# Kernel tuning notes

Hardware: AMD Instinct MI355X
Metric: run time of the kernel (lower is better)

## Reference

```python
import jax, jax.numpy as jnp
import numpy as np

B, L, D = 4, 2048, 256
H, DH, MLP, MAX_REL = 8, 32, 1024, 16
LN_EPS = 1e-5


def _layernorm(x, g, b):
    mu = jnp.mean(x, axis=-1, keepdims=True)
    var = jnp.mean(jnp.square(x - mu), axis=-1, keepdims=True)
    return (x - mu) * jax.lax.rsqrt(var + LN_EPS) * g + b


def setup_inputs() -> dict:
    key = jax.random.key(0)
    ks = jax.random.split(key, 16)
    s = 0.02
    return {
        "x": jax.random.normal(ks[0], (B, L, D), jnp.float32),
        "key_padding_mask": jax.random.randint(ks[1], (B, L), 0, 2).astype(bool),
        "Wqkv": jax.random.normal(ks[2], (D, 3 * D), jnp.float32) * s,
        "bqkv": jnp.zeros((3 * D,), jnp.float32),
        "Wo": jax.random.normal(ks[3], (D, D), jnp.float32) * s,
        "bo": jnp.zeros((D,), jnp.float32),
        "ln1_g": jnp.ones((D,), jnp.float32),
        "ln1_b": jnp.zeros((D,), jnp.float32),
        "W1": jax.random.normal(ks[4], (D, MLP), jnp.float32) * s,
        "b1": jnp.zeros((MLP,), jnp.float32),
        "W2": jax.random.normal(ks[5], (MLP, D), jnp.float32) * s,
        "b2": jnp.zeros((D,), jnp.float32),
        "ln2_g": jnp.ones((D,), jnp.float32),
        "ln2_b": jnp.zeros((D,), jnp.float32),
        "rel_bias": jax.random.normal(ks[6], (2 * MAX_REL + 1, H), jnp.float32) * 0.01,
    }


def reference(x, key_padding_mask, Wqkv, bqkv, Wo, bo, ln1_g, ln1_b,
              W1, b1, W2, b2, ln2_g, ln2_b, rel_bias):
    Bx, Lw, Dm = x.shape
    scale = DH ** -0.5
    qkv = x @ Wqkv + bqkv                                   # [B,L,3D]
    q, k, v = jnp.split(qkv, 3, axis=-1)
    q = q.reshape(Bx, Lw, H, DH).transpose(0, 2, 1, 3)      # [B,H,L,dh]
    k = k.reshape(Bx, Lw, H, DH).transpose(0, 2, 1, 3)
    v = v.reshape(Bx, Lw, H, DH).transpose(0, 2, 1, 3)
    scores = jnp.einsum("bhqd,bhkd->bhqk", q, k) * scale    # [B,H,L,L]
    idx = jnp.arange(Lw)
    rel_clip = jnp.clip(idx[None, :] - idx[:, None], -MAX_REL, MAX_REL) + MAX_REL
    bias = rel_bias[rel_clip].transpose(2, 0, 1)            # [H,L,L]
    scores = scores + bias[None]
    scores = jnp.where(key_padding_mask[:, None, None, :], jnp.float32(-1e9), scores)
    attn = jax.nn.softmax(scores, axis=-1)                  # dropout = identity (eval)
    out = jnp.einsum("bhqk,bhkd->bhqd", attn, v)
    out = out.transpose(0, 2, 1, 3).reshape(Bx, Lw, Dm)
    out = out @ Wo + bo
    x = _layernorm(x + out, ln1_g, ln1_b)
    m = jax.nn.relu(x @ W1 + b1) @ W2 + b2
    x = _layernorm(x + m, ln2_g, ln2_b)
    return x
```

## Files before the change

kernel.cpp:

```cpp
#include <hip/hip_runtime.h>

#define B_   4
#define L_   2048
#define D_   256
#define H_   8
#define DH_  32
#define MLP_ 1024
#define LOG2E 1.4426950408889634f

typedef __attribute__((ext_vector_type(8))) short  short8;
typedef __attribute__((ext_vector_type(4))) float  f32x4;
typedef __attribute__((ext_vector_type(2))) float  f32x2;
typedef unsigned long long ull;

union FragU { short8 v; struct { ull lo, hi; } q; unsigned u[4]; };
union SU { f32x4 v4; f32x2 v2[2]; };

__device__ __forceinline__ unsigned short f2bf(float f) {
  unsigned u = __float_as_uint(f);
  u += 0x7fffu + ((u >> 16) & 1u);
  return (unsigned short)(u >> 16);
}

__device__ __forceinline__ ull pack4(float a, float b, float c, float d) {
  return (ull)f2bf(a) | ((ull)f2bf(b) << 16) | ((ull)f2bf(c) << 32) | ((ull)f2bf(d) << 48);
}

__device__ __forceinline__ unsigned cvt_pk_bf16(float lo, float hi) {
  unsigned r;
  asm("v_cvt_pk_bf16_f32 %0, %1, %2" : "=v"(r) : "v"(lo), "v"(hi));
  return r;
}

__device__ __forceinline__ f32x2 pk_add(f32x2 a, f32x2 b) {
  f32x2 r; asm("v_pk_add_f32 %0, %1, %2" : "=v"(r) : "v"(a), "v"(b)); return r;
}

__device__ __forceinline__ float fexp2(float x) {
#if __has_builtin(__builtin_amdgcn_exp2f)
  return __builtin_amdgcn_exp2f(x);
#else
  return exp2f(x);
#endif
}

#define GLL16(gp, lp) __builtin_amdgcn_global_load_lds( \
    (const __attribute__((address_space(1))) void*)(gp), \
    (__attribute__((address_space(3))) void*)(lp), 16, 0, 0)

__global__ void prep_w(const float* __restrict__ x,
                       const float* __restrict__ Wqkv, const float* __restrict__ Wo,
                       const float* __restrict__ W1, const float* __restrict__ W2,
                       const int* __restrict__ mask, const float* __restrict__ relb,
                       unsigned short* __restrict__ xb,
                       unsigned short* __restrict__ wqkvt, unsigned short* __restrict__ wot,
                       unsigned short* __restrict__ w1t, unsigned short* __restrict__ w2t,
                       float* __restrict__ maskf,
                       float* __restrict__ mlo, float* __restrict__ mhi) {
  const int i = blockIdx.x * 256 + threadIdx.x;
  if (i < 524288) {
    const float4 v = *(const float4*)(x + (size_t)i * 4);
    *(ull*)(xb + (size_t)i * 4) = pack4(v.x, v.y, v.z, v.w);
  } else if (i < 720896) {
    const int j = i - 524288, r = j / 768, c = j - r * 768;
    wqkvt[(size_t)c * 256 + r] = f2bf(Wqkv[j]);
  } else if (i < 786432) {
    const int j = i - 720896, r = j >> 8, c = j & 255;
    wot[(size_t)c * 256 + r] = f2bf(Wo[j]);
  } else if (i < 1048576) {
    const int j = i - 786432, r = j >> 10, c = j & 1023;
    w1t[(size_t)c * 256 + r] = f2bf(W1[j]);
  } else if (i < 1310720) {
    const int j = i - 1048576, r = j >> 8, c = j & 255;
    w2t[(size_t)c * 1024 + r] = f2bf(W2[j]);
  } else if (i < 1318912) {
    const int j = i - 1310720;
    maskf[j] = mask[j] ? -1e9f : 0.f;
  } else {
    const int j2 = i - 1318912;
    const int t = j2 >> 16, idx = j2 & 65535;
    const int bh = idx >> 11, j = idx & 2047;
    const int bq = bh >> 3, h = bh & 7;
    const float base = mask[bq * L_ + j] ? -1e9f : 0.f;
    const float bias = relb[(t ? 32 * H_ : 0) + h] * LOG2E;
    (t ? mhi : mlo)[idx] = base + bias;
  }
}

template <int MODE, int TM, int TN, int NBX, int BYG>
__launch_bounds__(256)
__global__ void gemm_k(const unsigned short* __restrict__ A,
                       const unsigned short* __restrict__ Bt,
                       const float* __restrict__ bias,
                       unsigned short* __restrict__ outb0,
                       unsigned short* __restrict__ outb1,
                       unsigned short* __restrict__ outb2,
                       int K)
{
  constexpr int MI = TM / 32, NI = TN / 32;
  __shared__ alignas(16) unsigned short As[2][TM * 64];
  __shared__ alignas(16) unsigned short Bs[2][TN * 64];
  const int tid  = threadIdx.x;
  const int lane = tid & 63, wv = tid >> 6;
  const int wr = wv >> 1, wc = wv & 1;
  const int lr = lane & 15, g = lane >> 4;
  const int bid = blockIdx.x;
  const int xcd = bid & 7, ii = bid >> 3;
  const int by = xcd * BYG + ii / NBX;
  const int bx = ii % NBX;
  const int m0 = by * TM, n0 = bx * TN;
  const int l8 = lane >> 3, jj = lane & 7;

  auto stage = [&](int buf, int k0) {
#pragma unroll
    for (int i = 0; i < MI; ++i) {
      const int row = i * 32 + wv * 8 + l8;
      GLL16(A + (size_t)(m0 + row) * K + k0 + ((jj ^ (row & 7)) * 8),
            &As[buf][i * 2048 + wv * 512]);
    }
#pragma unroll
    for (int i = 0; i < NI; ++i) {
      const int row = i * 32 + wv * 8 + l8;
      GLL16(Bt + (size_t)(n0 + row) * K + k0 + ((jj ^ (row & 7)) * 8),
            &Bs[buf][i * 2048 + wv * 512]);
    }
  };

  f32x4 acc[MI][NI];
#pragma unroll
  for (int i = 0; i < MI; ++i)
#pragma unroll
    for (int j = 0; j < NI; ++j) acc[i][j] = (f32x4)(0.f);

  stage(0, 0);
  for (int k0 = 0; k0 < K; k0 += 64) {
    const int cur = (k0 >> 6) & 1;
    if (k0 + 64 < K) {
      stage(cur ^ 1, k0 + 64);
      asm volatile("s_waitcnt vmcnt(%0)" :: "n"(MI + NI) : "memory");
    } else {
      asm volatile("s_waitcnt vmcnt(0)" ::: "memory");
    }
    __builtin_amdgcn_sched_barrier(0);
    __builtin_amdgcn_s_barrier();
#pragma unroll
    for (int kk = 0; kk < 2; ++kk) {
      FragU af[MI], bf[NI];
#pragma unroll
      for (int mi = 0; mi < MI; ++mi) {
        const int row = wr * (TM / 2) + mi * 16 + lr;
        const int sw = (row & 7) << 3;
        af[mi].q.lo = *(const ull*)&As[cur][row * 64 + ((kk * 32 + 4 * g) ^ sw)];
        af[mi].q.hi = *(const ull*)&As[cur][row * 64 + ((kk * 32 + 16 + 4 * g) ^ sw)];
      }
#pragma unroll
      for (int ni = 0; ni < NI; ++ni) {
        const int row = wc * (TN / 2) + ni * 16 + lr;
        const int sw = (row & 7) << 3;
        bf[ni].q.lo = *(const ull*)&Bs[cur][row * 64 + ((kk * 32 + 4 * g) ^ sw)];
        bf[ni].q.hi = *(const ull*)&Bs[cur][row * 64 + ((kk * 32 + 16 + 4 * g) ^ sw)];
      }
#pragma unroll
      for (int mi = 0; mi < MI; ++mi)
#pragma unroll
        for (int ni = 0; ni < NI; ++ni)
          acc[mi][ni] = __builtin_amdgcn_mfma_f32_16x16x32_bf16(af[mi].v, bf[ni].v, acc[mi][ni], 0, 0, 0);
    }
    asm volatile("s_waitcnt lgkmcnt(0)" ::: "memory");
    __builtin_amdgcn_sched_barrier(0);
    __builtin_amdgcn_s_barrier();
  }

#pragma unroll
  for (int mi = 0; mi < MI; ++mi) {
#pragma unroll
    for (int ni = 0; ni < NI; ++ni) {
      const int n = n0 + wc * (TN / 2) + ni * 16 + lr;
      const float bv = bias[n];
#pragma unroll
      for (int r = 0; r < 4; ++r) {
        const int m = m0 + wr * (TM / 2) + mi * 16 + 4 * g + r;
        float val = acc[mi][ni][r] + bv;
        if constexpr (MODE == 0) {
          const int s = n >> 8, hh = (n >> 5) & 7, dh = n & 31;
          const int bb = m >> 11, l = m & (L_ - 1);
          if (s == 0) {
            outb0[((size_t)(bb * H_ + hh) * L_ + l) * DH_ + dh] =
                f2bf(val * (0.17677669529663687f * LOG2E));
          } else if (s == 1) {
            outb1[((size_t)(bb * H_ + hh) * L_ + l) * DH_ + dh] = f2bf(val);
          } else {
            outb2[((size_t)(bb * H_ + hh) * DH_ + dh) * L_ + l] = f2bf(val);
          }
        } else {
          outb0[(size_t)m * MLP_ + n] = f2bf(fmaxf(val, 0.f));
        }
      }
    }
  }
}

template <bool WRITE_BF>
__launch_bounds__(512)
__global__ void gemmln_k(const unsigned short* __restrict__ A,
                         const unsigned short* __restrict__ Bt,
                         const float* __restrict__ bias,
                         const float* __restrict__ resid,
                         const float* __restrict__ lng,
                         const float* __restrict__ lnb,
                         float* __restrict__ outf,
                         unsigned short* __restrict__ outb,
                         int K)
{
  __shared__ alignas(16) unsigned short As[2][16 * 64];
  __shared__ alignas(16) unsigned short Bs[2][256 * 64];
  __shared__ float rsum[8][16], rsq[8][16], rmu[16], rrstd[16];
  const int tid  = threadIdx.x;
  const int lane = tid & 63, wv = tid >> 6;
  const int lr = lane & 15, g = lane >> 4;
  const int m0 = blockIdx.x * 16;
  const int l8 = lane >> 3, jj = lane & 7;

  auto stage = [&](int buf, int k0) {
    if (wv < 2) {
      const int row = wv * 8 + l8;
      GLL16(A + (size_t)(m0 + row) * K + k0 + ((jj ^ (row & 7)) * 8),
            &As[buf][wv * 512]);
    }
#pragma unroll
    for (int i = 0; i < 4; ++i) {
      const int n = i * 64 + wv * 8 + l8;
      GLL16(Bt + (size_t)n * K + k0 + ((jj ^ (n & 7)) * 8),
            &Bs[buf][i * 4096 + wv * 512]);
    }
  };

  f32x4 acc[2];
  acc[0] = (f32x4)(0.f); acc[1] = (f32x4)(0.f);

  stage(0, 0);
  for (int k0 = 0; k0 < K; k0 += 64) {
    const int cur = (k0 >> 6) & 1;
    if (k0 + 64 < K) {
      stage(cur ^ 1, k0 + 64);
      asm volatile("s_waitcnt vmcnt(4)" ::: "memory");
    } else {
      asm volatile("s_waitcnt vmcnt(0)" ::: "memory");
    }
    __builtin_amdgcn_sched_barrier(0);
    __builtin_amdgcn_s_barrier();
#pragma unroll
    for (int kk = 0; kk < 2; ++kk) {
      FragU af, bf[2];
      {
        const int sw = (lr & 7) << 3;
        af.q.lo = *(const ull*)&As[cur][lr * 64 + ((kk * 32 + 4 * g) ^ sw)];
        af.q.hi = *(const ull*)&As[cur][lr * 64 + ((kk * 32 + 16 + 4 * g) ^ sw)];
      }
#pragma unroll
      for (int ni = 0; ni < 2; ++ni) {
        const int row = wv * 32 + ni * 16 + lr;
        const int sw = (row & 7) << 3;
        bf[ni].q.lo = *(const ull*)&Bs[cur][row * 64 + ((kk * 32 + 4 * g) ^ sw)];
        bf[ni].q.hi = *(const ull*)&Bs[cur][row * 64 + ((kk * 32 + 16 + 4 * g) ^ sw)];
      }
#pragma unroll
      for (int ni = 0; ni < 2; ++ni)
        acc[ni] = __builtin_amdgcn_mfma_f32_16x16x32_bf16(af.v, bf[ni].v, acc[ni], 0, 0, 0);
    }
    asm volatile("s_waitcnt lgkmcnt(0)" ::: "memory");
    __builtin_amdgcn_sched_barrier(0);
    __builtin_amdgcn_s_barrier();
  }

  float g2[2], b2[2], bias2[2];
  int col[2];
#pragma unroll
  for (int ni = 0; ni < 2; ++ni) {
    col[ni] = wv * 32 + ni * 16 + lr;
    g2[ni] = lng[col[ni]]; b2[ni] = lnb[col[ni]]; bias2[ni] = bias[col[ni]];
  }
  float vals[2][4];
#pragma unroll
  for (int r = 0; r < 4; ++r) {
    const int row = 4 * g + r;
    float s = 0.f, q = 0.f;
#pragma unroll
    for (int ni = 0; ni < 2; ++ni) {
      float v = acc[ni][r] + bias2[ni] + resid[(size_t)(m0 + row) * D_ + col[ni]];
      vals[ni][r] = v; s += v; q += v * v;
    }
#pragma unroll
    for (int off = 1; off < 16; off <<= 1) {
      s += __shfl_xor(s, off); q += __shfl_xor(q, off);
    }
    if (lr == 0) { rsum[wv][row] = s; rsq[wv][row] = q; }
  }
  __syncthreads();
  if (tid < 16) {
    float s = 0.f, q = 0.f;
#pragma unroll
    for (int w = 0; w < 8; ++w) { s += rsum[w][tid]; q += rsq[w][tid]; }
    const float mu = s * (1.f / D_);
    rmu[tid] = mu;
    rrstd[tid] = rsqrtf(q * (1.f / D_) - mu * mu + 1e-5f);
  }
  __syncthreads();
#pragma unroll
  for (int r = 0; r < 4; ++r) {
    const int row = 4 * g + r;
    const float mu = rmu[row], rs = rrstd[row];
#pragma unroll
    for (int ni = 0; ni < 2; ++ni) {
      const float o = (vals[ni][r] - mu) * rs * g2[ni] + b2[ni];
      const size_t idx = (size_t)(m0 + row) * D_ + col[ni];
      outf[idx] = o;
      if constexpr (WRITE_BF) outb[idx] = f2bf(o);
    }
  }
}

__launch_bounds__(256, 4)
__global__ void attn_k(const unsigned short* __restrict__ qb,
                       const unsigned short* __restrict__ kp,
                       const unsigned short* __restrict__ vT,
                       const float* __restrict__ maskf,
                       const float* __restrict__ mlo,
                       const float* __restrict__ mhi,
                       const float* __restrict__ relb,
                       unsigned short* __restrict__ aout)
{
  __shared__ alignas(16) unsigned short Ks[2][128 * 40];
  __shared__ alignas(16) unsigned short Vs[2][32 * 128];
  __shared__ alignas(16) float biasv[36];
  const int tid = threadIdx.x;
  const int lane = tid & 63, wv = tid >> 6;
  const int lr = lane & 15, g = lane >> 4;
  const int bid = blockIdx.x;
  const int ii = bid >> 3;
  const int bh = (bid & 7) * 4 + (ii >> 5);
  const int qblk = ii & 31;
  const int b = bh >> 3, h = bh & 7;
  const size_t bhoff = (size_t)bh * (L_ * DH_);
  if (tid < 33) biasv[tid] = relb[tid * H_ + h] * LOG2E;
  const int qw0 = qblk * 64 + wv * 16;

  FragU qf;
  {
    const unsigned short* qr = qb + bhoff + (size_t)(qw0 + lr) * DH_;
    qf.q.lo = *(const ull*)(qr + 4 * g);
    qf.q.hi = *(const ull*)(qr + 16 + 4 * g);
  }
  f32x4 O0 = (f32x4)(0.f), O1 = (f32x4)(0.f);
  f32x2 ssum2 = {0.f, 0.f};
  const f32x4 z4 = (f32x4)(0.f);
  const int krow = tid >> 1, koff = (tid & 1) * 16;
  const float* mtl = mlo + (size_t)bh * L_ + 4 * g;
  const float* mth = mhi + (size_t)bh * L_ + 4 * g;
  const float* mbn = maskf + (size_t)b * L_ + 4 * g;

  {
    const unsigned short* ksrc = kp + bhoff + (size_t)krow * DH_ + koff;
    const int4 ka = *(const int4*)ksrc;
    const int4 kc = *(const int4*)(ksrc + 8);
#pragma unroll
    for (int i = 0; i < 2; ++i) {
      const int d = (wv * 2 + i) * 4 + (lane >> 4);
      GLL16(vT + ((size_t)bh * DH_ + d) * L_ + (((lane & 15) * 8) ^ ((d & 7) * 8)),
            &Vs[0][(wv * 2 + i) * 512]);
    }
    *(int4*)&Ks[0][krow * 40 + koff] = ka;
    *(int4*)&Ks[0][krow * 40 + koff + 8] = kc;
    asm volatile("s_waitcnt vmcnt(0) lgkmcnt(0)" ::: "memory");
    __builtin_amdgcn_s_barrier();
  }

#pragma unroll 2
  for (int ch = 0; ch < 16; ++ch) {
    const int cur = ch & 1, nxt = cur ^ 1;
    const int kv = ch * 128;
    const bool more = ch < 15;
    int4 ka = {0, 0, 0, 0}, kc = {0, 0, 0, 0};
    if (more) {
      const unsigned short* ksrc = kp + bhoff + (size_t)(kv + 128 + krow) * DH_ + koff;
      ka = *(const int4*)ksrc;
      kc = *(const int4*)(ksrc + 8);
#pragma unroll
      for (int i = 0; i < 2; ++i) {
        const int d = (wv * 2 + i) * 4 + (lane >> 4);
        GLL16(vT + ((size_t)bh * DH_ + d) * L_ + kv + 128 + (((lane & 15) * 8) ^ ((d & 7) * 8)),
              &Vs[nxt][(wv * 2 + i) * 512]);
      }
    }

    SU sT[2][4];
#pragma unroll
    for (int st = 0; st < 2; ++st) {
      const unsigned short* KsC = &Ks[cur][st * 64 * 40];
#pragma unroll
      for (int jt = 0; jt < 4; ++jt) {
        FragU kf;
        const int base = (jt * 16 + lr) * 40;
        kf.q.lo = *(const ull*)&KsC[base + 4 * g];
        kf.q.hi = *(const ull*)&KsC[base + 16 + 4 * g];
        sT[st][jt].v4 = __builtin_amdgcn_mfma_f32_16x16x32_bf16(kf.v, qf.v, z4, 0, 0, 0);
      }
    }

#pragma unroll
    for (int st = 0; st < 2; ++st) {
      const int j0 = kv + st * 64;
      const int dlt = j0 - qw0;
      if (dlt >= 32 || dlt <= -80) {
        const float* mt = (dlt > 0) ? mth : mtl;
#pragma unroll
        for (int jt = 0; jt < 4; ++jt) {
          SU mk; mk.v4 = *(const f32x4*)(mt + j0 + jt * 16);
          sT[st][jt].v2[0] = pk_add(sT[st][jt].v2[0], mk.v2[0]);
          sT[st][jt].v2[1] = pk_add(sT[st][jt].v2[1], mk.v2[1]);
        }
      } else {
#pragma unroll
        for (int jt = 0; jt < 4; ++jt)
#pragma unroll
          for (int r = 0; r < 4; ++r) {
            int rel = j0 + jt * 16 + 4 * g + r - (qw0 + lr);
            rel = rel < -16 ? -16 : (rel > 16 ? 16 : rel);
            sT[st][jt].v4[r] += biasv[rel + 16] + mbn[j0 + jt * 16 + r];
          }
      }
#pragma unroll
      for (int jt = 0; jt < 4; ++jt)
#pragma unroll
        for (int r = 0; r < 4; ++r)
          sT[st][jt].v4[r] = fexp2(sT[st][jt].v4[r]);
      const f32x2 s01 = pk_add(sT[st][0].v2[0], sT[st][0].v2[1]);
      const f32x2 s23 = pk_add(sT[st][1].v2[0], sT[st][1].v2[1]);
      const f32x2 s45 = pk_add(sT[st][2].v2[0], sT[st][2].v2[1]);
      const f32x2 s67 = pk_add(sT[st][3].v2[0], sT[st][3].v2[1]);
      ssum2 = pk_add(ssum2, pk_add(pk_add(s01, s23), pk_add(s45, s67)));

      FragU a0, a1;
      a0.u[0] = cvt_pk_bf16(sT[st][0].v4[0], sT[st][0].v4[1]);
      a0.u[1] = cvt_pk_bf16(sT[st][0].v4[2], sT[st][0].v4[3]);
      a0.u[2] = cvt_pk_bf16(sT[st][1].v4[0], sT[st][1].v4[1]);
      a0.u[3] = cvt_pk_bf16(sT[st][1].v4[2], sT[st][1].v4[3]);
      a1.u[0] = cvt_pk_bf16(sT[st][2].v4[0], sT[st][2].v4[1]);
      a1.u[1] = cvt_pk_bf16(sT[st][2].v4[2], sT[st][2].v4[3]);
      a1.u[2] = cvt_pk_bf16(sT[st][3].v4[0], sT[st][3].v4[1]);
      a1.u[3] = cvt_pk_bf16(sT[st][3].v4[2], sT[st][3].v4[3]);

      FragU vf00, vf01, vf10, vf11;
#pragma unroll
      for (int dt = 0; dt < 2; ++dt) {
        const int row = dt * 16 + lr;
        const int sw = (row & 7) << 3;
        FragU v0, v1;
        v0.q.lo = *(const ull*)&Vs[cur][row * 128 + ((st * 64 + 4 * g) ^ sw)];
        v0.q.hi = *(const ull*)&Vs[cur][row * 128 + ((st * 64 + 16 + 4 * g) ^ sw)];
        v1.q.lo = *(const ull*)&Vs[cur][row * 128 + ((st * 64 + 32 + 4 * g) ^ sw)];
        v1.q.hi = *(const ull*)&Vs[cur][row * 128 + ((st * 64 + 48 + 4 * g) ^ sw)];
        if (dt == 0) { vf00 = v0; vf01 = v1; } else { vf10 = v0; vf11 = v1; }
      }
      O0 = __builtin_amdgcn_mfma_f32_16x16x32_bf16(a0.v, vf00.v, O0, 0, 0, 0);
      O0 = __builtin_amdgcn_mfma_f32_16x16x32_bf16(a1.v, vf01.v, O0, 0, 0, 0);
      O1 = __builtin_amdgcn_mfma_f32_16x16x32_bf16(a0.v, vf10.v, O1, 0, 0, 0);
      O1 = __builtin_amdgcn_mfma_f32_16x16x32_bf16(a1.v, vf11.v, O1, 0, 0, 0);
    }

    if (more) {
      *(int4*)&Ks[nxt][krow * 40 + koff] = ka;
      *(int4*)&Ks[nxt][krow * 40 + koff + 8] = kc;
    }
    asm volatile("s_waitcnt vmcnt(0) lgkmcnt(0)" ::: "memory");
    __builtin_amdgcn_sched_barrier(0);
    __builtin_amdgcn_s_barrier();
  }

  float ssum = ssum2[0] + ssum2[1];
  ssum += __shfl_xor(ssum, 16);
  ssum += __shfl_xor(ssum, 32);
#pragma unroll
  for (int r = 0; r < 4; ++r) {
    const float sden = __shfl(ssum, 4 * g + r);
    const float inv = 1.f / sden;
    const int qo = qw0 + 4 * g + r;
    unsigned short* orow = aout + ((size_t)(b * L_ + qo)) * D_ + h * DH_;
    orow[lr]      = f2bf(O0[r] * inv);
    orow[16 + lr] = f2bf(O1[r] * inv);
  }
}

extern "C" void kernel_launch(void* const* d_in, const int* in_sizes, int n_in,
                              void* d_out, int out_size, void* d_ws, size_t ws_size,
                              hipStream_t stream) {
  (void)in_sizes; (void)n_in; (void)out_size; (void)ws_size;
  const float* x    = (const float*)d_in[0];
  const int*   mask = (const int*)d_in[1];
  const float* Wqkv = (const float*)d_in[2];
  const float* bqkv = (const float*)d_in[3];
  const float* Wo   = (const float*)d_in[4];
  const float* bo   = (const float*)d_in[5];
  const float* ln1g = (const float*)d_in[6];
  const float* ln1b = (const float*)d_in[7];
  const float* W1   = (const float*)d_in[8];
  const float* b1   = (const float*)d_in[9];
  const float* W2   = (const float*)d_in[10];
  const float* b2   = (const float*)d_in[11];
  const float* ln2g = (const float*)d_in[12];
  const float* ln2b = (const float*)d_in[13];
  const float* relb = (const float*)d_in[14];

  size_t off = 0;
  char* wsb = (char*)d_ws;
  auto carve = [&](size_t bytes) -> void* {
    void* p = wsb + off;
    off += (bytes + 255) & ~(size_t)255;
    return p;
  };
  const size_t tokb = (size_t)B_ * L_;
  unsigned short* xb    = (unsigned short*)carve(tokb * D_ * 2);
  unsigned short* qbuf  = (unsigned short*)carve(tokb * D_ * 2);
  unsigned short* kbuf  = (unsigned short*)carve(tokb * D_ * 2);
  unsigned short* vTb   = (unsigned short*)carve(tokb * D_ * 2);
  unsigned short* attnb = (unsigned short*)carve(tokb * D_ * 2);
  unsigned short* wqkvt = (unsigned short*)carve((size_t)3 * D_ * D_ * 2);
  unsigned short* wot   = (unsigned short*)carve((size_t)D_ * D_ * 2);
  unsigned short* w1t   = (unsigned short*)carve((size_t)D_ * MLP_ * 2);
  unsigned short* w2t   = (unsigned short*)carve((size_t)D_ * MLP_ * 2);
  float*          x1    = (float*)carve(tokb * D_ * 4);
  unsigned short* x1b   = (unsigned short*)carve(tokb * D_ * 2);
  unsigned short* hbuf  = (unsigned short*)carve(tokb * MLP_ * 2);
  float*          maskfb = (float*)carve(tokb * 4);
  float*          mlob  = (float*)carve((size_t)B_ * H_ * L_ * 4);
  float*          mhib  = (float*)carve((size_t)B_ * H_ * L_ * 4);

  prep_w<<<5664, 256, 0, stream>>>(x, Wqkv, Wo, W1, W2, mask, relb,
                                   xb, wqkvt, wot, w1t, w2t, maskfb, mlob, mhib);

  gemm_k<0, 64, 128, 6, 16><<<768, 256, 0, stream>>>(
      xb, wqkvt, bqkv, qbuf, kbuf, vTb, D_);
  attn_k<<<1024, 256, 0, stream>>>(
      qbuf, kbuf, vTb, maskfb, mlob, mhib, relb, attnb);
  gemmln_k<true><<<tokb / 16, 512, 0, stream>>>(
      attnb, wot, bo, x, ln1g, ln1b, x1, x1b, D_);
  gemm_k<2, 64, 128, 8, 16><<<1024, 256, 0, stream>>>(
      x1b, w1t, b1, hbuf, nullptr, nullptr, D_);
  gemmln_k<false><<<tokb / 16, 512, 0, stream>>>(
      hbuf, w2t, b2, x1, ln2g, ln2b, (float*)d_out, nullptr, MLP_);
}
```

Baseline: 113.5 us.

## Replace LDS-staged double buffering in GEMM+LayerNorm with direct global fragment loads

```diff
diff --git a/kernel.cpp b/kernel.cpp
--- a/kernel.cpp
+++ b/kernel.cpp
@@ -200,7 +200,7 @@
   }
 }
 
-template <bool WRITE_BF>
+template <bool WRITE_BF, int K>
 __launch_bounds__(512)
 __global__ void gemmln_k(const unsigned short* __restrict__ A,
                          const unsigned short* __restrict__ Bt,
@@ -209,68 +209,29 @@
                          const float* __restrict__ lng,
                          const float* __restrict__ lnb,
                          float* __restrict__ outf,
-                         unsigned short* __restrict__ outb,
-                         int K)
+                         unsigned short* __restrict__ outb)
 {
-  __shared__ alignas(16) unsigned short As[2][16 * 64];
-  __shared__ alignas(16) unsigned short Bs[2][256 * 64];
   __shared__ float rsum[8][16], rsq[8][16], rmu[16], rrstd[16];
   const int tid  = threadIdx.x;
   const int lane = tid & 63, wv = tid >> 6;
   const int lr = lane & 15, g = lane >> 4;
   const int m0 = blockIdx.x * 16;
-  const int l8 = lane >> 3, jj = lane & 7;
-
-  auto stage = [&](int buf, int k0) {
-    if (wv < 2) {
-      const int row = wv * 8 + l8;
-      GLL16(A + (size_t)(m0 + row) * K + k0 + ((jj ^ (row & 7)) * 8),
-            &As[buf][wv * 512]);
-    }
-#pragma unroll
-    for (int i = 0; i < 4; ++i) {
-      const int n = i * 64 + wv * 8 + l8;
-      GLL16(Bt + (size_t)n * K + k0 + ((jj ^ (n & 7)) * 8),
-            &Bs[buf][i * 4096 + wv * 512]);
-    }
-  };
+
+  const unsigned short* ar  = A  + (size_t)(m0 + lr) * K + 8 * g;
+  const unsigned short* br0 = Bt + (size_t)(wv * 32 + lr) * K + 8 * g;
+  const unsigned short* br1 = br0 + (size_t)16 * K;
 
   f32x4 acc[2];
   acc[0] = (f32x4)(0.f); acc[1] = (f32x4)(0.f);
 
-  stage(0, 0);
-  for (int k0 = 0; k0 < K; k0 += 64) {
-    const int cur = (k0 >> 6) & 1;
-    if (k0 + 64 < K) {
-      stage(cur ^ 1, k0 + 64);
-      asm volatile("s_waitcnt vmcnt(4)" ::: "memory");
-    } else {
-      asm volatile("s_waitcnt vmcnt(0)" ::: "memory");
-    }
-    __builtin_amdgcn_sched_barrier(0);
-    __builtin_amdgcn_s_barrier();
-#pragma unroll
-    for (int kk = 0; kk < 2; ++kk) {
-      FragU af, bf[2];
-      {
-        const int sw = (lr & 7) << 3;
-        af.q.lo = *(const ull*)&As[cur][lr * 64 + ((kk * 32 + 4 * g) ^ sw)];
-        af.q.hi = *(const ull*)&As[cur][lr * 64 + ((kk * 32 + 16 + 4 * g) ^ sw)];
-      }
-#pragma unroll
-      for (int ni = 0; ni < 2; ++ni) {
-        const int row = wv * 32 + ni * 16 + lr;
-        const int sw = (row & 7) << 3;
-        bf[ni].q.lo = *(const ull*)&Bs[cur][row * 64 + ((kk * 32 + 4 * g) ^ sw)];
-        bf[ni].q.hi = *(const ull*)&Bs[cur][row * 64 + ((kk * 32 + 16 + 4 * g) ^ sw)];
-      }
-#pragma unroll
-      for (int ni = 0; ni < 2; ++ni)
-        acc[ni] = __builtin_amdgcn_mfma_f32_16x16x32_bf16(af.v, bf[ni].v, acc[ni], 0, 0, 0);
-    }
-    asm volatile("s_waitcnt lgkmcnt(0)" ::: "memory");
-    __builtin_amdgcn_sched_barrier(0);
-    __builtin_amdgcn_s_barrier();
+#pragma unroll 8
+  for (int k0 = 0; k0 < K; k0 += 32) {
+    FragU af, b0, b1;
+    af.v = *(const short8*)(ar + k0);
+    b0.v = *(const short8*)(br0 + k0);
+    b1.v = *(const short8*)(br1 + k0);
+    acc[0] = __builtin_amdgcn_mfma_f32_16x16x32_bf16(af.v, b0.v, acc[0], 0, 0, 0);
+    acc[1] = __builtin_amdgcn_mfma_f32_16x16x32_bf16(af.v, b1.v, acc[1], 0, 0, 0);
   }
 
   float g2[2], b2[2], bias2[2];
@@ -542,10 +503,10 @@
       xb, wqkvt, bqkv, qbuf, kbuf, vTb, D_);
   attn_k<<<1024, 256, 0, stream>>>(
       qbuf, kbuf, vTb, maskfb, mlob, mhib, relb, attnb);
-  gemmln_k<true><<<tokb / 16, 512, 0, stream>>>(
-      attnb, wot, bo, x, ln1g, ln1b, x1, x1b, D_);
+  gemmln_k<true, D_><<<tokb / 16, 512, 0, stream>>>(
+      attnb, wot, bo, x, ln1g, ln1b, x1, x1b);
   gemm_k<2, 64, 128, 8, 16><<<1024, 256, 0, stream>>>(
       x1b, w1t, b1, hbuf, nullptr, nullptr, D_);
-  gemmln_k<false><<<tokb / 16, 512, 0, stream>>>(
-      hbuf, w2t, b2, x1, ln2g, ln2b, (float*)d_out, nullptr, MLP_);
-}
+  gemmln_k<false, MLP_><<<tokb / 16, 512, 0, stream>>>(
+      hbuf, w2t, b2, x1, ln2g, ln2b, (float*)d_out, nullptr);
+}
```

Result: slower. 146.7 us (+29.3%).
